# Kernel optimization log

Measured on AMD Instinct MI355X. Metric: run time of the kernel, lower is better.

The kernel has to match this reference:

```python
import jax, jax.numpy as jnp
import numpy as np

B, S, D = 8, 1024, 512          # batch, seq_len, d_model
H, HD = 8, 64                   # num_heads, head_dim (D = H*HD)
L = 128                         # latent_dim
LH = L // H                     # latent_head_dim = 16
M_ALPHA = -1e9                  # additive mask coefficient


def setup_inputs() -> dict:
    key = jax.random.key(0)
    ks = jax.random.split(key, 9)
    s = 0.02
    return {
        "x": jax.random.normal(ks[0], (B, S, D), jnp.float32),
        "mask": jax.random.uniform(ks[1], (B, S, 1), jnp.float32),  # (B,S,1) single-column mask
        "Wq": jax.random.normal(ks[2], (D, D), jnp.float32) * s,
        "bq": jnp.zeros((D,), jnp.float32),
        "Wckv": jax.random.normal(ks[3], (D, L), jnp.float32) * s,   # latent KV compression
        "Wuk": jax.random.normal(ks[4], (L, D), jnp.float32) * s,    # key up-proj (absorbed into q)
        "Wuv": jax.random.normal(ks[5], (L, D), jnp.float32) * s,    # value up-proj
        "Wo": jax.random.normal(ks[6], (D, D), jnp.float32) * s,
        "bo": jnp.zeros((D,), jnp.float32),
    }


def reference(x, mask, Wq, bq, Wckv, Wuk, Wuv, Wo, bo):
    b, s, d = x.shape
    # Q path: full query then project into latent space via Wuk^T (weight absorption)
    q_full = x @ Wq + bq                              # (B,S,D)
    q_lat = q_full @ Wuk.T                            # (B,S,L)
    q = q_lat.reshape(b, s, H, LH).transpose(0, 2, 1, 3)      # (B,H,S,LH)
    # K/V path: compressed latent KV
    k_lat_full = x @ Wckv                             # (B,S,L)
    k = k_lat_full.reshape(b, s, H, LH).transpose(0, 2, 1, 3)  # (B,H,S,LH)
    v_full = k_lat_full @ Wuv                         # (B,S,D)
    v = v_full.reshape(b, s, H, HD).transpose(0, 2, 1, 3)      # (B,H,S,HD)
    # scaled dot-product in latent space (dk = latent_head_dim)
    logits = jnp.einsum('bhqd,bhkd->bhqk', q, k) / jnp.sqrt(jnp.float32(LH))
    qk_values = logits
    # 'QK' mask: tile single-column (B,S,1)->(B,S,S), symmetrize, clamp at 1
    m = jnp.broadcast_to(mask, (b, s, s))             # tile along keys
    m = m + m.transpose(0, 2, 1)                      # symmetric (square case)
    m = jnp.minimum(1.0, m)
    logits = logits + m[:, None, :, :] * M_ALPHA      # (B,H,S,S)
    attn_weights = jax.nn.softmax(logits, axis=-1)
    attn = jnp.einsum('bhqk,bhkd->bhqd', attn_weights, v)      # (B,H,S,HD)
    attn = attn.transpose(0, 2, 1, 3).reshape(b, s, d)         # merge heads
    out = attn @ Wo + bo                              # (B,S,D)
    return out, attn_weights, qk_values
```

## Files before the change

### kernel.cpp

```cpp
#include <hip/hip_runtime.h>
#include <hip/hip_bf16.h>

typedef __hip_bfloat16 bf16;
typedef __attribute__((ext_vector_type(8))) short short8;
typedef __attribute__((ext_vector_type(4))) float f32x4;

#define B_ 8
#define S_ 1024
#define D_ 512
#define H_ 8
#define HD_ 64
#define L_ 128
#define LH_ 16

__device__ __forceinline__ float bfu2f(unsigned short u) {
  unsigned int x = ((unsigned int)u) << 16;
  float f;
  __builtin_memcpy(&f, &x, 4);
  return f;
}
__device__ __forceinline__ unsigned short bfbits(float f) {
  bf16 h = __float2bfloat16(f);
  unsigned short u;
  __builtin_memcpy(&u, &h, 2);
  return u;
}
__device__ __forceinline__ f32x4 mfma_bf16(short8 a, short8 b, f32x4 c) {
  return __builtin_amdgcn_mfma_f32_16x16x32_bf16(a, b, c, 0, 0, 0);
}

template<bool BT, bool BIAS, bool ABF16, bool CBF16>
__global__ __launch_bounds__(256) void gemm(const void* __restrict__ Ap, int lda,
                                            const void* __restrict__ Bp, int ldb,
                                            void* __restrict__ Cp, int ldc,
                                            const float* __restrict__ bias, int K) {
  __shared__ float As[16][65];
  __shared__ float Bs[16][65];
  const int tid = threadIdx.x;
  const int m0 = blockIdx.y * 64, n0 = blockIdx.x * 64;
  const int ty = tid >> 4, tx = tid & 15;
  float acc[4][4] = {};
  for (int kt = 0; kt < K; kt += 16) {
    {
      const int m = tid >> 2, kq = (tid & 3) * 4;
      if (ABF16) {
        const bf16* A = (const bf16*)Ap;
        ushort4 u = *reinterpret_cast<const ushort4*>(
            reinterpret_cast<const unsigned short*>(A) + (size_t)(m0 + m) * lda + kt + kq);
        As[kq + 0][m] = bfu2f(u.x);
        As[kq + 1][m] = bfu2f(u.y);
        As[kq + 2][m] = bfu2f(u.z);
        As[kq + 3][m] = bfu2f(u.w);
      } else {
        const float* A = (const float*)Ap;
        float4 v = *reinterpret_cast<const float4*>(A + (size_t)(m0 + m) * lda + kt + kq);
        As[kq + 0][m] = v.x;
        As[kq + 1][m] = v.y;
        As[kq + 2][m] = v.z;
        As[kq + 3][m] = v.w;
      }
    }
    if (BT) {
      const int n = tid >> 2, kq = (tid & 3) * 4;
      const float* Bf = (const float*)Bp;
      float4 v = *reinterpret_cast<const float4*>(Bf + (size_t)(n0 + n) * ldb + kt + kq);
      Bs[kq + 0][n] = v.x;
      Bs[kq + 1][n] = v.y;
      Bs[kq + 2][n] = v.z;
      Bs[kq + 3][n] = v.w;
    } else {
      const int k = tid >> 4, nq = (tid & 15) * 4;
      const float* Bf = (const float*)Bp;
      float4 v = *reinterpret_cast<const float4*>(Bf + (size_t)(kt + k) * ldb + n0 + nq);
      Bs[k][nq + 0] = v.x;
      Bs[k][nq + 1] = v.y;
      Bs[k][nq + 2] = v.z;
      Bs[k][nq + 3] = v.w;
    }
    __syncthreads();
#pragma unroll
    for (int k = 0; k < 16; ++k) {
      float a0 = As[k][ty * 4 + 0], a1 = As[k][ty * 4 + 1];
      float a2 = As[k][ty * 4 + 2], a3 = As[k][ty * 4 + 3];
      float b0 = Bs[k][tx * 4 + 0], b1 = Bs[k][tx * 4 + 1];
      float b2 = Bs[k][tx * 4 + 2], b3 = Bs[k][tx * 4 + 3];
      acc[0][0] += a0 * b0; acc[0][1] += a0 * b1; acc[0][2] += a0 * b2; acc[0][3] += a0 * b3;
      acc[1][0] += a1 * b0; acc[1][1] += a1 * b1; acc[1][2] += a1 * b2; acc[1][3] += a1 * b3;
      acc[2][0] += a2 * b0; acc[2][1] += a2 * b1; acc[2][2] += a2 * b2; acc[2][3] += a2 * b3;
      acc[3][0] += a3 * b0; acc[3][1] += a3 * b1; acc[3][2] += a3 * b2; acc[3][3] += a3 * b3;
    }
    __syncthreads();
  }
#pragma unroll
  for (int i = 0; i < 4; ++i)
#pragma unroll
    for (int j = 0; j < 4; ++j) {
      const size_t row = m0 + ty * 4 + i;
      const int col = n0 + tx * 4 + j;
      float v = acc[i][j];
      if (BIAS) v += bias[col];
      if (CBF16)
        reinterpret_cast<bf16*>(Cp)[row * ldc + col] = __float2bfloat16(v);
      else
        reinterpret_cast<float*>(Cp)[row * ldc + col] = v;
    }
}

__global__ __launch_bounds__(256) void k_tr_f32(const float* __restrict__ in,
                                                float* __restrict__ out, int R, int C) {
  __shared__ float t[32][33];
  int tx = threadIdx.x & 31, ty = threadIdx.x >> 5;
  int r0 = blockIdx.y * 32, c0 = blockIdx.x * 32;
#pragma unroll
  for (int i = 0; i < 32; i += 8)
    t[ty + i][tx] = in[(size_t)(r0 + ty + i) * C + c0 + tx];
  __syncthreads();
#pragma unroll
  for (int i = 0; i < 32; i += 8)
    out[(size_t)(c0 + ty + i) * R + r0 + tx] = t[tx][ty + i];
}

__global__ __launch_bounds__(256) void k_tr_f32_bf16(const float* __restrict__ in,
                                                     bf16* __restrict__ out,
                                                     int R, int C) {
  __shared__ float t[32][33];
  int tx = threadIdx.x & 31, ty = threadIdx.x >> 5;
  int r0 = blockIdx.y * 32, c0 = blockIdx.x * 32;
#pragma unroll
  for (int i = 0; i < 32; i += 8)
    t[ty + i][tx] = in[(size_t)(r0 + ty + i) * C + c0 + tx];
  __syncthreads();
#pragma unroll
  for (int i = 0; i < 32; i += 8)
    out[(size_t)(c0 + ty + i) * R + r0 + tx] = __float2bfloat16(t[tx][ty + i]);
}

__global__ __launch_bounds__(256) void k_copy_wckv(const float* __restrict__ Wckv,
                                                   float* __restrict__ wcat) {
  int idx = blockIdx.x * 256 + threadIdx.x;
  int k = idx >> 7, n = idx & 127;
  wcat[k * 256 + 128 + n] = Wckv[k * 128 + n];
}

__global__ __launch_bounds__(64) void k_biascomb(const float* __restrict__ bq,
                                                 const float* __restrict__ Wuk,
                                                 float* __restrict__ bias_c) {
  int j = blockIdx.x, lane = threadIdx.x;
  if (j >= L_) { if (lane == 0) bias_c[j] = 0.f; return; }
  float s = 0.f;
  for (int d = lane; d < D_; d += 64) s += bq[d] * Wuk[j * D_ + d];
#pragma unroll
  for (int off = 32; off > 0; off >>= 1) s += __shfl_down(s, off);
  if (lane == 0) bias_c[j] = s;
}

__global__ __launch_bounds__(256) void k_qk3(const float* __restrict__ xw,
                                             const float* __restrict__ maskg,
                                             float* __restrict__ qk_out,
                                             float* __restrict__ aw_out) {
  __shared__ __align__(16) float Kl[512 * 20];
  __shared__ float mkl[S_];
  __shared__ float qls[8 * 16];
  const int bh = blockIdx.y, b = bh >> 3, h = bh & 7;
  const int q0 = blockIdx.x * 8;
  const int tid = threadIdx.x, w = tid >> 6, lane = tid & 63;

  for (int i = tid; i < S_; i += 256) mkl[i] = maskg[b * S_ + i];
  if (tid < 32) {
    const int row = tid >> 2, qq = (tid & 3) * 4;
    float4 v = *reinterpret_cast<const float4*>(
        xw + (size_t)(b * S_ + q0 + row) * 256 + h * LH_ + qq);
    qls[row * 16 + qq + 0] = v.x; qls[row * 16 + qq + 1] = v.y;
    qls[row * 16 + qq + 2] = v.z; qls[row * 16 + qq + 3] = v.w;
  }
  __syncthreads();

  const int r0 = w * 2;
  float qr[2][16], mq[2];
#pragma unroll
  for (int r = 0; r < 2; ++r) {
#pragma unroll
    for (int t = 0; t < 16; ++t) qr[r][t] = qls[(r0 + r) * 16 + t];
    mq[r] = mkl[q0 + r0 + r];
  }
  const size_t obase = (size_t)bh * S_ * S_;
  float l[2][16];

#pragma unroll
  for (int half = 0; half < 2; ++half) {
    if (half) __syncthreads();
#pragma unroll
    for (int i = 0; i < 8; ++i) {
      const int idx = tid + i * 256;
      const int key = idx >> 2, qq = (idx & 3) * 4;
      float4 v = *reinterpret_cast<const float4*>(
          xw + (size_t)(b * S_ + half * 512 + key) * 256 + 128 + h * LH_ + qq);
      *reinterpret_cast<float4*>(&Kl[key * 20 + qq]) = v;
    }
    __syncthreads();
#pragma unroll
    for (int c = 0; c < 8; ++c) {
      const int lkey = c * 64 + lane;
      const int key = half * 512 + lkey;
      float kv[16];
#pragma unroll
      for (int t = 0; t < 16; t += 4) {
        float4 v = *reinterpret_cast<const float4*>(&Kl[lkey * 20 + t]);
        kv[t] = v.x; kv[t + 1] = v.y; kv[t + 2] = v.z; kv[t + 3] = v.w;
      }
      const float mk = mkl[key];
#pragma unroll
      for (int r = 0; r < 2; ++r) {
        float d = 0.f;
#pragma unroll
        for (int t = 0; t < 16; ++t) d += qr[r][t] * kv[t];
        d *= 0.25f;
        qk_out[obase + (size_t)(q0 + r0 + r) * S_ + key] = d;
        const float m = fminf(1.f, __fadd_rn(mq[r], mk));
        l[r][half * 8 + c] = __fadd_rn(d, __fmul_rn(m, -1e9f));
      }
    }
  }

#pragma unroll
  for (int r = 0; r < 2; ++r) {
    float M = l[r][0];
#pragma unroll
    for (int idx = 1; idx < 16; ++idx) M = fmaxf(M, l[r][idx]);
#pragma unroll
    for (int st = 1; st < 64; st <<= 1) M = fmaxf(M, __shfl_xor(M, st));
    float s = 0.f;
#pragma unroll
    for (int idx = 0; idx < 16; ++idx) {
      const float e = __expf(l[r][idx] - M);
      l[r][idx] = e;
      s += e;
    }
#pragma unroll
    for (int st = 1; st < 64; st <<= 1) s += __shfl_xor(s, st);
    const float inv = 1.f / s;
    const size_t orow = obase + (size_t)(q0 + r0 + r) * S_;
#pragma unroll
    for (int idx = 0; idx < 16; ++idx)
      aw_out[orow + (idx >> 3) * 512 + (idx & 7) * 64 + lane] = l[r][idx] * inv;
  }
}

__global__ __launch_bounds__(256) void k_pv_mfma(const float* __restrict__ aw,
                                                 const bf16* __restrict__ vt,
                                                 bf16* __restrict__ attn) {
  __shared__ __align__(16) short Pl[128 * 40];
  __shared__ __align__(16) short Vl[64 * 40];
  const int bh = blockIdx.y, b = bh >> 3, h = bh & 7;
  const int q0 = blockIdx.x * 128;
  const int tid = threadIdx.x, w = tid >> 6, lane = tid & 63;
  const int l15 = lane & 15, l4 = lane >> 4;
  const float* A = aw + (size_t)bh * S_ * S_;
  const unsigned short* vtp =
      reinterpret_cast<const unsigned short*>(vt) + (size_t)h * 64 * 8192 + b * S_;
  f32x4 acc[2][4] = {};
  for (int kt = 0; kt < 32; ++kt) {
    __syncthreads();
    {
      const int r = tid >> 1, half = (tid & 1) * 16;
      const float* src = A + (size_t)(q0 + r) * S_ + kt * 32 + half;
      short* dst = &Pl[r * 40 + half];
#pragma unroll
      for (int i = 0; i < 4; ++i) {
        float4 v = *reinterpret_cast<const float4*>(src + i * 4);
        ushort4 o = { bfbits(v.x), bfbits(v.y), bfbits(v.z), bfbits(v.w) };
        *reinterpret_cast<ushort4*>(dst + i * 4) = o;
      }
    }
    if (tid < 64) {
      const unsigned short* src = vtp + (size_t)tid * 8192 + kt * 32;
      *reinterpret_cast<uint4*>(&Vl[tid * 40 + 0])  = *reinterpret_cast<const uint4*>(src + 0);
      *reinterpret_cast<uint4*>(&Vl[tid * 40 + 8])  = *reinterpret_cast<const uint4*>(src + 8);
      *reinterpret_cast<uint4*>(&Vl[tid * 40 + 16]) = *reinterpret_cast<const uint4*>(src + 16);
      *reinterpret_cast<uint4*>(&Vl[tid * 40 + 24]) = *reinterpret_cast<const uint4*>(src + 24);
    }
    __syncthreads();
    short8 av[2], bv[4];
#pragma unroll
    for (int mf = 0; mf < 2; ++mf)
      av[mf] = *reinterpret_cast<const short8*>(&Pl[(w * 32 + mf * 16 + l15) * 40 + l4 * 8]);
#pragma unroll
    for (int nf = 0; nf < 4; ++nf)
      bv[nf] = *reinterpret_cast<const short8*>(&Vl[(nf * 16 + l15) * 40 + l4 * 8]);
#pragma unroll
    for (int mf = 0; mf < 2; ++mf)
#pragma unroll
      for (int nf = 0; nf < 4; ++nf)
        acc[mf][nf] = mfma_bf16(av[mf], bv[nf], acc[mf][nf]);
  }
#pragma unroll
  for (int mf = 0; mf < 2; ++mf)
#pragma unroll
    for (int nf = 0; nf < 4; ++nf)
#pragma unroll
      for (int j = 0; j < 4; ++j)
        attn[(size_t)(b * S_ + q0 + w * 32 + mf * 16 + l4 * 4 + j) * 512 +
             h * 64 + nf * 16 + l15] = __float2bfloat16(acc[mf][nf][j]);
}

__global__ __launch_bounds__(256) void gemm_mfma_out(const bf16* __restrict__ Ab,
                                                     const bf16* __restrict__ Bt,
                                                     float* __restrict__ C,
                                                     const float* __restrict__ bias) {
  __shared__ __align__(16) short sA[128 * 40];
  __shared__ __align__(16) short sB[128 * 40];
  const int tid = threadIdx.x, lane = tid & 63;
  const int l15 = lane & 15, l4 = lane >> 4;
  const int wm = ((tid >> 6) >> 1) * 64, wn = ((tid >> 6) & 1) * 64;
  const size_t bn0 = (size_t)blockIdx.x * 128, bm0 = (size_t)blockIdx.y * 128;
  const unsigned short* A = reinterpret_cast<const unsigned short*>(Ab);
  const unsigned short* Bu = reinterpret_cast<const unsigned short*>(Bt);
  f32x4 acc[4][4] = {};
  for (int kt = 0; kt < 512; kt += 32) {
    __syncthreads();
#pragma unroll
    for (int i = 0; i < 2; ++i) {
      const int c = tid + i * 256;
      const int row = c >> 2, k8 = (c & 3) * 8;
      *reinterpret_cast<uint4*>(&sA[row * 40 + k8]) =
          *reinterpret_cast<const uint4*>(A + (bm0 + row) * 512 + kt + k8);
      *reinterpret_cast<uint4*>(&sB[row * 40 + k8]) =
          *reinterpret_cast<const uint4*>(Bu + (bn0 + row) * 512 + kt + k8);
    }
    __syncthreads();
    short8 av[4], bv[4];
#pragma unroll
    for (int mf = 0; mf < 4; ++mf)
      av[mf] = *reinterpret_cast<const short8*>(&sA[(wm + mf * 16 + l15) * 40 + l4 * 8]);
#pragma unroll
    for (int nf = 0; nf < 4; ++nf)
      bv[nf] = *reinterpret_cast<const short8*>(&sB[(wn + nf * 16 + l15) * 40 + l4 * 8]);
#pragma unroll
    for (int mf = 0; mf < 4; ++mf)
#pragma unroll
      for (int nf = 0; nf < 4; ++nf)
        acc[mf][nf] = mfma_bf16(av[mf], bv[nf], acc[mf][nf]);
  }
#pragma unroll
  for (int mf = 0; mf < 4; ++mf)
#pragma unroll
    for (int nf = 0; nf < 4; ++nf)
#pragma unroll
      for (int j = 0; j < 4; ++j) {
        const size_t row = bm0 + wm + mf * 16 + l4 * 4 + j;
        const int col = bn0 + wn + nf * 16 + l15;
        C[row * 512 + col] = acc[mf][nf][j] + bias[col];
      }
}

extern "C" void kernel_launch(void* const* d_in, const int* in_sizes, int n_in,
                              void* d_out, int out_size, void* d_ws, size_t ws_size,
                              hipStream_t stream) {
  const float* x    = (const float*)d_in[0];
  const float* mask = (const float*)d_in[1];
  const float* Wq   = (const float*)d_in[2];
  const float* bq   = (const float*)d_in[3];
  const float* Wckv = (const float*)d_in[4];
  const float* Wuk  = (const float*)d_in[5];
  const float* Wuv  = (const float*)d_in[6];
  const float* Wo   = (const float*)d_in[7];
  const float* bo   = (const float*)d_in[8];

  float* out    = (float*)d_out;
  float* aw_out = out + (size_t)B_ * S_ * D_;
  float* qk_out = aw_out + (size_t)B_ * H_ * S_ * S_;

  uint8_t* p = (uint8_t*)d_ws;
  auto alloc = [&](size_t bytes) {
    void* r = p;
    p += (bytes + 255) & ~(size_t)255;
    return r;
  };
  float* wcat    = (float*)alloc((size_t)512 * 256 * 4);
  float* bias_c  = (float*)alloc(256 * 4);
  float* wuvT_f  = (float*)alloc((size_t)512 * 128 * 4);
  bf16*  woT     = (bf16*)alloc((size_t)512 * 512 * 2);
  float* xw      = (float*)alloc((size_t)8192 * 256 * 4);
  bf16*  vt      = (bf16*)alloc((size_t)512 * 8192 * 2);
  bf16*  attn_bf = (bf16*)xw;

  gemm<true, false, false, false><<<dim3(2, 8), 256, 0, stream>>>(
      Wq, 512, Wuk, 512, wcat, 256, nullptr, 512);
  k_copy_wckv<<<256, 256, 0, stream>>>(Wckv, wcat);
  k_biascomb<<<256, 64, 0, stream>>>(bq, Wuk, bias_c);
  k_tr_f32<<<dim3(16, 4), 256, 0, stream>>>(Wuv, wuvT_f, 128, 512);
  k_tr_f32_bf16<<<dim3(16, 16), 256, 0, stream>>>(Wo, woT, 512, 512);
  gemm<false, true, false, false><<<dim3(4, 128), 256, 0, stream>>>(
      x, 512, wcat, 256, xw, 256, bias_c, 512);
  gemm<true, false, false, true><<<dim3(128, 8), 256, 0, stream>>>(
      wuvT_f, 128, xw + 128, 256, vt, 8192, nullptr, 128);
  k_qk3<<<dim3(128, 64), 256, 0, stream>>>(xw, mask, qk_out, aw_out);
  k_pv_mfma<<<dim3(8, 64), 256, 0, stream>>>(aw_out, vt, attn_bf);
  gemm_mfma_out<<<dim3(4, 64), 256, 0, stream>>>(attn_bf, woT, out, bo);
  (void)in_sizes; (void)n_in; (void)out_size; (void)ws_size;
}
```

Baseline: 374.1 us.

## Compute QK logits with bf16 MFMA and two-sweep bounded softmax

Replaces the scalar fp32 QK/softmax kernel with one that computes Q·K on bf16 MFMA tiles of 128 query rows per block. A new pre-pass kernel computes, per batch-head, the maximum key norm and minimum mask value. These give a Cauchy-Schwarz upper bound on each row's max logit, so no row-max reduction is needed. Softmax then runs in two sweeps over keys, recomputing the MFMA: one sweep writes qk and accumulates the exp-sum, the other writes normalized weights. This trades fp32 accuracy of qk_values for bf16-rounded inputs, doubles the QK compute, and produces narrower 64-byte store segments; exp may underflow if the bound is loose.

After: 380.2 us. About the same (+1.6%).

```diff
diff --git a/kernel.cpp b/kernel.cpp
--- a/kernel.cpp
+++ b/kernel.cpp
@@ -28,6 +28,7 @@
 __device__ __forceinline__ f32x4 mfma_bf16(short8 a, short8 b, f32x4 c) {
   return __builtin_amdgcn_mfma_f32_16x16x32_bf16(a, b, c, 0, 0, 0);
 }
+
 
 template<bool BT, bool BIAS, bool ABF16, bool CBF16>
 __global__ __launch_bounds__(256) void gemm(const void* __restrict__ Ap, int lda,
@@ -154,95 +155,167 @@
   if (lane == 0) bias_c[j] = s;
 }
 
-__global__ __launch_bounds__(256) void k_qk3(const float* __restrict__ xw,
-                                             const float* __restrict__ maskg,
-                                             float* __restrict__ qk_out,
-                                             float* __restrict__ aw_out) {
-  __shared__ __align__(16) float Kl[512 * 20];
+__global__ __launch_bounds__(256) void k_stats(const float* __restrict__ xw,
+                                               const float* __restrict__ maskg,
+                                               float* __restrict__ kmaxg,
+                                               float* __restrict__ mkming) {
+  __shared__ float rk[256], rm[256];
+  const int bh = blockIdx.x, b = bh >> 3, h = bh & 7;
+  const int tid = threadIdx.x;
+  float kmax2 = 0.f, mmin = 1e30f;
+#pragma unroll
+  for (int i = 0; i < 4; ++i) {
+    const int key = tid + i * 256;
+    const float* src = xw + (size_t)(b * S_ + key) * 256 + 128 + h * 16;
+    float n2 = 0.f;
+#pragma unroll
+    for (int t = 0; t < 16; t += 4) {
+      float4 v = *reinterpret_cast<const float4*>(src + t);
+      float c0 = bfu2f(bfbits(v.x)), c1 = bfu2f(bfbits(v.y));
+      float c2 = bfu2f(bfbits(v.z)), c3 = bfu2f(bfbits(v.w));
+      n2 += c0 * c0 + c1 * c1 + c2 * c2 + c3 * c3;
+    }
+    kmax2 = fmaxf(kmax2, n2);
+    mmin = fminf(mmin, maskg[b * S_ + key]);
+  }
+  rk[tid] = kmax2;
+  rm[tid] = mmin;
+  __syncthreads();
+  for (int s = 128; s > 0; s >>= 1) {
+    if (tid < s) {
+      rk[tid] = fmaxf(rk[tid], rk[tid + s]);
+      rm[tid] = fminf(rm[tid], rm[tid + s]);
+    }
+    __syncthreads();
+  }
+  if (tid == 0) {
+    kmaxg[bh] = sqrtf(rk[0]);
+    mkming[bh] = rm[0];
+  }
+}
+
+__global__ __launch_bounds__(256) void k_qk_mf(const float* __restrict__ xw,
+                                               const float* __restrict__ maskg,
+                                               const float* __restrict__ kmaxg,
+                                               const float* __restrict__ mkming,
+                                               float* __restrict__ qk_out,
+                                               float* __restrict__ aw_out) {
+  __shared__ __align__(16) short Ql[128 * 40];
+  __shared__ __align__(16) short Kl[512 * 40];
   __shared__ float mkl[S_];
-  __shared__ float qls[8 * 16];
+  __shared__ float qn[128];
   const int bh = blockIdx.y, b = bh >> 3, h = bh & 7;
-  const int q0 = blockIdx.x * 8;
+  const int q0 = blockIdx.x * 128;
   const int tid = threadIdx.x, w = tid >> 6, lane = tid & 63;
+  const int l15 = lane & 15, l4 = lane >> 4;
 
   for (int i = tid; i < S_; i += 256) mkl[i] = maskg[b * S_ + i];
-  if (tid < 32) {
-    const int row = tid >> 2, qq = (tid & 3) * 4;
-    float4 v = *reinterpret_cast<const float4*>(
-        xw + (size_t)(b * S_ + q0 + row) * 256 + h * LH_ + qq);
-    qls[row * 16 + qq + 0] = v.x; qls[row * 16 + qq + 1] = v.y;
-    qls[row * 16 + qq + 2] = v.z; qls[row * 16 + qq + 3] = v.w;
+
+  {
+    const int row = tid >> 1, ks = (tid & 1) * 16;
+    short* dst = &Ql[row * 40 + ks];
+    if (ks == 0) {
+      const float* src = xw + (size_t)(b * S_ + q0 + row) * 256 + h * 16;
+      float n2 = 0.f;
+#pragma unroll
+      for (int t = 0; t < 16; t += 4) {
+        float4 v = *reinterpret_cast<const float4*>(src + t);
+        ushort4 o = { bfbits(v.x), bfbits(v.y), bfbits(v.z), bfbits(v.w) };
+        *reinterpret_cast<ushort4*>(dst + t) = o;
+        float c0 = bfu2f(o.x), c1 = bfu2f(o.y), c2 = bfu2f(o.z), c3 = bfu2f(o.w);
+        n2 += c0 * c0 + c1 * c1 + c2 * c2 + c3 * c3;
+      }
+      qn[row] = sqrtf(n2);
+    } else {
+      uint4 zz = { 0, 0, 0, 0 };
+      *reinterpret_cast<uint4*>(dst + 0) = zz;
+      *reinterpret_cast<uint4*>(dst + 8) = zz;
+    }
   }
   __syncthreads();
 
-  const int r0 = w * 2;
-  float qr[2][16], mq[2];
-#pragma unroll
-  for (int r = 0; r < 2; ++r) {
-#pragma unroll
-    for (int t = 0; t < 16; ++t) qr[r][t] = qls[(r0 + r) * 16 + t];
-    mq[r] = mkl[q0 + r0 + r];
-  }
+  short8 aq[2];
+#pragma unroll
+  for (int mf = 0; mf < 2; ++mf)
+    aq[mf] = *reinterpret_cast<const short8*>(&Ql[(w * 32 + mf * 16 + l15) * 40 + l4 * 8]);
+
+  const float kmax = kmaxg[bh], mkmin = mkming[bh];
+  float mq[2][4], Mub[2][4], sm[2][4];
+#pragma unroll
+  for (int mf = 0; mf < 2; ++mf)
+#pragma unroll
+    for (int j = 0; j < 4; ++j) {
+      const int rl = w * 32 + mf * 16 + l4 * 4 + j;
+      mq[mf][j] = mkl[q0 + rl];
+      Mub[mf][j] = __fmul_rn(fminf(1.f, __fadd_rn(mq[mf][j], mkmin)), -1e9f) +
+                   0.25f * qn[rl] * kmax + 0.5f;
+      sm[mf][j] = 0.f;
+    }
+
   const size_t obase = (size_t)bh * S_ * S_;
-  float l[2][16];
-
-#pragma unroll
-  for (int half = 0; half < 2; ++half) {
-    if (half) __syncthreads();
-#pragma unroll
-    for (int i = 0; i < 8; ++i) {
-      const int idx = tid + i * 256;
-      const int key = idx >> 2, qq = (idx & 3) * 4;
-      float4 v = *reinterpret_cast<const float4*>(
-          xw + (size_t)(b * S_ + half * 512 + key) * 256 + 128 + h * LH_ + qq);
-      *reinterpret_cast<float4*>(&Kl[key * 20 + qq]) = v;
-    }
-    __syncthreads();
-#pragma unroll
-    for (int c = 0; c < 8; ++c) {
-      const int lkey = c * 64 + lane;
-      const int key = half * 512 + lkey;
-      float kv[16];
-#pragma unroll
-      for (int t = 0; t < 16; t += 4) {
-        float4 v = *reinterpret_cast<const float4*>(&Kl[lkey * 20 + t]);
-        kv[t] = v.x; kv[t + 1] = v.y; kv[t + 2] = v.z; kv[t + 3] = v.w;
-      }
-      const float mk = mkl[key];
-#pragma unroll
-      for (int r = 0; r < 2; ++r) {
-        float d = 0.f;
-#pragma unroll
-        for (int t = 0; t < 16; ++t) d += qr[r][t] * kv[t];
-        d *= 0.25f;
-        qk_out[obase + (size_t)(q0 + r0 + r) * S_ + key] = d;
-        const float m = fminf(1.f, __fadd_rn(mq[r], mk));
-        l[r][half * 8 + c] = __fadd_rn(d, __fmul_rn(m, -1e9f));
-      }
-    }
-  }
-
-#pragma unroll
-  for (int r = 0; r < 2; ++r) {
-    float M = l[r][0];
-#pragma unroll
-    for (int idx = 1; idx < 16; ++idx) M = fmaxf(M, l[r][idx]);
-#pragma unroll
-    for (int st = 1; st < 64; st <<= 1) M = fmaxf(M, __shfl_xor(M, st));
-    float s = 0.f;
-#pragma unroll
-    for (int idx = 0; idx < 16; ++idx) {
-      const float e = __expf(l[r][idx] - M);
-      l[r][idx] = e;
-      s += e;
-    }
-#pragma unroll
-    for (int st = 1; st < 64; st <<= 1) s += __shfl_xor(s, st);
-    const float inv = 1.f / s;
-    const size_t orow = obase + (size_t)(q0 + r0 + r) * S_;
-#pragma unroll
-    for (int idx = 0; idx < 16; ++idx)
-      aw_out[orow + (idx >> 3) * 512 + (idx & 7) * 64 + lane] = l[r][idx] * inv;
+#pragma unroll
+  for (int sweep = 0; sweep < 2; ++sweep) {
+    for (int half = 0; half < 2; ++half) {
+      __syncthreads();
+#pragma unroll
+      for (int i = 0; i < 4; ++i) {
+        const int unit = tid + i * 256;
+        const int key = unit >> 1, ks = (unit & 1) * 16;
+        short* dst = &Kl[key * 40 + ks];
+        if (ks == 0) {
+          const float* src = xw + (size_t)(b * S_ + half * 512 + key) * 256 + 128 + h * 16;
+#pragma unroll
+          for (int t = 0; t < 16; t += 4) {
+            float4 v = *reinterpret_cast<const float4*>(src + t);
+            ushort4 o = { bfbits(v.x), bfbits(v.y), bfbits(v.z), bfbits(v.w) };
+            *reinterpret_cast<ushort4*>(dst + t) = o;
+          }
+        } else {
+          uint4 zz = { 0, 0, 0, 0 };
+          *reinterpret_cast<uint4*>(dst + 0) = zz;
+          *reinterpret_cast<uint4*>(dst + 8) = zz;
+        }
+      }
+      __syncthreads();
+      for (int c = 0; c < 32; ++c) {
+        const int lkey = c * 16 + l15;
+        const int key = half * 512 + lkey;
+        const short8 bk = *reinterpret_cast<const short8*>(&Kl[lkey * 40 + l4 * 8]);
+        const float mk = mkl[key];
+#pragma unroll
+        for (int mf = 0; mf < 2; ++mf) {
+          f32x4 z = {};
+          f32x4 s4 = mfma_bf16(aq[mf], bk, z);
+#pragma unroll
+          for (int j = 0; j < 4; ++j) {
+            const float qk = s4[j] * 0.25f;
+            const int qrow = q0 + w * 32 + mf * 16 + l4 * 4 + j;
+            const float m = fminf(1.f, __fadd_rn(mq[mf][j], mk));
+            const float l = __fadd_rn(qk, __fmul_rn(m, -1e9f));
+            if (sweep == 0) {
+              qk_out[obase + (size_t)qrow * S_ + key] = qk;
+              sm[mf][j] += __expf(l - Mub[mf][j]);
+            } else {
+              aw_out[obase + (size_t)qrow * S_ + key] =
+                  __expf(l - Mub[mf][j]) * sm[mf][j];
+            }
+          }
+        }
+      }
+    }
+    if (sweep == 0) {
+#pragma unroll
+      for (int mf = 0; mf < 2; ++mf)
+#pragma unroll
+        for (int j = 0; j < 4; ++j) {
+          float s = sm[mf][j];
+          s += __shfl_xor(s, 1);
+          s += __shfl_xor(s, 2);
+          s += __shfl_xor(s, 4);
+          s += __shfl_xor(s, 8);
+          sm[mf][j] = 1.f / s;
+        }
+    }
   }
 }
 
@@ -380,6 +453,8 @@
   float* bias_c  = (float*)alloc(256 * 4);
   float* wuvT_f  = (float*)alloc((size_t)512 * 128 * 4);
   bf16*  woT     = (bf16*)alloc((size_t)512 * 512 * 2);
+  float* kmaxg   = (float*)alloc(64 * 4);
+  float* mkming  = (float*)alloc(64 * 4);
   float* xw      = (float*)alloc((size_t)8192 * 256 * 4);
   bf16*  vt      = (bf16*)alloc((size_t)512 * 8192 * 2);
   bf16*  attn_bf = (bf16*)xw;
@@ -394,7 +469,8 @@
       x, 512, wcat, 256, xw, 256, bias_c, 512);
   gemm<true, false, false, true><<<dim3(128, 8), 256, 0, stream>>>(
       wuvT_f, 128, xw + 128, 256, vt, 8192, nullptr, 128);
-  k_qk3<<<dim3(128, 64), 256, 0, stream>>>(xw, mask, qk_out, aw_out);
+  k_stats<<<64, 256, 0, stream>>>(xw, mask, kmaxg, mkming);
+  k_qk_mf<<<dim3(8, 64), 256, 0, stream>>>(xw, mask, kmaxg, mkming, qk_out, aw_out);
   k_pv_mfma<<<dim3(8, 64), 256, 0, stream>>>(aw_out, vt, attn_bf);
   gemm_mfma_out<<<dim3(4, 64), 256, 0, stream>>>(attn_bf, woT, out, bo);
   (void)in_sizes; (void)n_in; (void)out_size; (void)ws_size;
```
